# Optimization experiments

Hardware: AMD Instinct MI355X
Metric: run time of the kernel (lower is better)

The kernel has to match this reference:

```python
import jax, jax.numpy as jnp
import numpy as np

DIM = 1024
N_HEADS = 16
HEAD_DIM = DIM // N_HEADS


def setup_inputs() -> dict:
    key = jax.random.key(0)
    ks = jax.random.split(key, 7)
    B, S = 2, 2048
    scale = 0.02
    return {
        "q": jax.random.normal(ks[0], (B, S, DIM), dtype=jnp.float32),
        "k": jax.random.normal(ks[1], (B, S, DIM), dtype=jnp.float32),
        "v": jax.random.normal(ks[2], (B, S, DIM), dtype=jnp.float32),
        # torch nn.Linear weights are [out_features, in_features]; y = x @ W.T
        "wq": jax.random.normal(ks[3], (DIM, DIM), dtype=jnp.float32) * scale,
        "wk": jax.random.normal(ks[4], (DIM, DIM), dtype=jnp.float32) * scale,
        "wv": jax.random.normal(ks[5], (DIM, DIM), dtype=jnp.float32) * scale,
        "wo": jax.random.normal(ks[6], (DIM, DIM), dtype=jnp.float32) * scale,
    }


def reference(q, k, v, wq, wk, wv, wo):
    B, S, _ = q.shape
    H, D = N_HEADS, HEAD_DIM
    # projections (torch Linear: x @ W.T), reshape to [B, H, S, D]
    xq = (q @ wq.T).reshape(B, S, H, D).transpose(0, 2, 1, 3)
    xk = (k @ wk.T).reshape(B, S, H, D).transpose(0, 2, 1, 3)
    xv = (v @ wv.T).reshape(B, S, H, D).transpose(0, 2, 1, 3)
    # scaled dot-product attention with causal mask
    scores = jnp.einsum("bhqd,bhkd->bhqk", xq, xk) / jnp.sqrt(jnp.float32(D))
    causal = jnp.tril(jnp.ones((S, S), dtype=bool))
    scores = jnp.where(causal, scores, -jnp.inf)
    attn = jax.nn.softmax(scores.astype(jnp.float32), axis=-1).astype(xq.dtype)
    # dropout prob = 0.0 (eval-mode / deterministic reference)
    out = jnp.einsum("bhqk,bhkd->bhqd", attn, xv)
    out = out.transpose(0, 2, 1, 3).reshape(B, S, H * D)
    return out @ wo.T
```

## Files before the change

### kernel.cpp

```cpp
#include <hip/hip_runtime.h>
#include <hip/hip_bf16.h>
#include <stdint.h>


typedef short s16x8 __attribute__((ext_vector_type(8)));
typedef float f32x4 __attribute__((ext_vector_type(4)));

#define MFMA_BF16 __builtin_amdgcn_mfma_f32_16x16x32_bf16

static __device__ __forceinline__ unsigned short f2bf(float f) {
    union { float f; unsigned u; } x{f};
    unsigned r = x.u + 0x7fff + ((x.u >> 16) & 1);
    return (unsigned short)(r >> 16);
}
static __device__ __forceinline__ unsigned pk2h(float a, float b) {
    __hip_bfloat162 h = __float22bfloat162_rn(float2{a, b});
    return *(unsigned*)&h;
}

static __device__ __forceinline__ void ald16(unsigned short* lds, const unsigned short* g) {
    __builtin_amdgcn_global_load_lds(
        (const __attribute__((address_space(1))) unsigned int*)g,
        (__attribute__((address_space(3))) unsigned int*)lds, 16, 0, 0);
}

#define QSCL 0.18033688f

__global__ __launch_bounds__(256) void convert_all_kernel(
        const float* __restrict__ q, const float* __restrict__ k,
        const float* __restrict__ v,
        const float* __restrict__ wq, const float* __restrict__ wk,
        const float* __restrict__ wv, const float* __restrict__ wo,
        unsigned short* __restrict__ dst) {
    const size_t idx = ((size_t)blockIdx.x * 256 + threadIdx.x) * 8;
    const int region = (int)(idx >> 22);
    const float* src;
    size_t off;
    if (region == 0)      { src = q; off = idx; }
    else if (region == 1) { src = k; off = idx & 4194303; }
    else if (region == 2) { src = v; off = idx & 4194303; }
    else {
        const int wsel = (int)((idx >> 20) & 3);
        src = wsel == 0 ? wq : wsel == 1 ? wk : wsel == 2 ? wv : wo;
        off = idx & 1048575;
    }
    const float4* p = (const float4*)(src + off);
    float4 a = p[0], b = p[1];
    uint4 u;
    u.x = pk2h(a.x, a.y); u.y = pk2h(a.z, a.w);
    u.z = pk2h(b.x, b.y); u.w = pk2h(b.z, b.w);
    *(uint4*)(dst + idx) = u;
}

__global__ __launch_bounds__(256) void wconvert_kernel(
        const float* __restrict__ wq, const float* __restrict__ wk,
        const float* __restrict__ wv, const float* __restrict__ wo,
        unsigned short* __restrict__ Wb) {
    const size_t idx = ((size_t)blockIdx.x * 256 + threadIdx.x) * 8;
    const int region = (int)(idx >> 20);
    const size_t off = idx & 1048575;
    const float* src = region == 0 ? wq : region == 1 ? wk : region == 2 ? wv : wo;
    const float4* p = (const float4*)(src + off);
    float4 a = p[0], b = p[1];
    uint4 u;
    u.x = pk2h(a.x, a.y); u.y = pk2h(a.z, a.w);
    u.z = pk2h(b.x, b.y); u.w = pk2h(b.z, b.w);
    *(uint4*)(Wb + idx) = u;
}

__global__ __launch_bounds__(256) void proj3b_kernel(
        const unsigned short* __restrict__ Qb, const unsigned short* __restrict__ Kb,
        const unsigned short* __restrict__ Vb, const unsigned short* __restrict__ Wb,
        unsigned short* __restrict__ Xq, unsigned short* __restrict__ Xk,
        unsigned short* __restrict__ Xvt) {
    constexpr int Kd = 1024;
    __shared__ union {
        struct { unsigned short A[3][128 * 32]; unsigned short B[3][128 * 32]; } s;
        unsigned short T[4 * 64 * 68];
    } sm;

    const int z = blockIdx.z;
    const unsigned short* A  = z == 0 ? Qb : z == 1 ? Kb : Vb;
    const unsigned short* Bw = Wb + (size_t)z * 1048576;

    const int t = threadIdx.x;
    const int m0 = blockIdx.x * 128, n0 = blockIdx.y * 128;
    const int w = t >> 6, lane = t & 63, fr = lane & 15, g = lane >> 4;
    const int wm = (w >> 1) * 64, wn = (w & 1) * 64;
    const int brow = t >> 2;
    const int cB = (t & 3) ^ ((t >> 3) & 3);
    const int sB = g ^ ((fr >> 1) & 3);

    f32x4 acc[4][4] = {};

    auto STAGE = [&](int p, int kk) {
        ald16(sm.s.A[p] + (size_t)w * 512,        A  + (size_t)(m0 + brow) * Kd + kk + cB * 8);
        ald16(sm.s.A[p] + 2048 + (size_t)w * 512, A  + (size_t)(m0 + 64 + brow) * Kd + kk + cB * 8);
        ald16(sm.s.B[p] + (size_t)w * 512,        Bw + (size_t)(n0 + brow) * Kd + kk + cB * 8);
        ald16(sm.s.B[p] + 2048 + (size_t)w * 512, Bw + (size_t)(n0 + 64 + brow) * Kd + kk + cB * 8);
    };

    STAGE(0, 0);
    STAGE(1, 32);
    int bi = 0, nb = 2;

    for (int k0 = 0; k0 < Kd; k0 += 32) {
        if (k0 < Kd - 64) {
            STAGE(nb, k0 + 64);
            asm volatile("s_waitcnt vmcnt(8)" ::: "memory");
        } else if (k0 < Kd - 32) {
            asm volatile("s_waitcnt vmcnt(4)" ::: "memory");
        } else {
            asm volatile("s_waitcnt vmcnt(0)" ::: "memory");
        }
        __builtin_amdgcn_s_barrier();
        asm volatile("" ::: "memory");

        s16x8 af[4], bfv[4];
#pragma unroll
        for (int mi = 0; mi < 4; ++mi)
            af[mi] = *(const s16x8*)(sm.s.A[bi] + (wm + mi * 16 + fr) * 32 + sB * 8);
#pragma unroll
        for (int ni = 0; ni < 4; ++ni)
            bfv[ni] = *(const s16x8*)(sm.s.B[bi] + (wn + ni * 16 + fr) * 32 + sB * 8);
#pragma unroll
        for (int mi = 0; mi < 4; ++mi)
#pragma unroll
            for (int ni = 0; ni < 4; ++ni)
                acc[mi][ni] = MFMA_BF16(af[mi], bfv[ni], acc[mi][ni], 0, 0, 0);

        asm volatile("" ::: "memory");
        __builtin_amdgcn_s_barrier();
        bi = bi == 2 ? 0 : bi + 1;
        nb = nb == 2 ? 0 : nb + 1;
    }

    if (z != 2) {
        unsigned short* C = z ? Xk : Xq;
        const float osc = z == 0 ? QSCL : 1.0f;
#pragma unroll
        for (int mi = 0; mi < 4; ++mi)
#pragma unroll
            for (int ni = 0; ni < 4; ++ni)
#pragma unroll
                for (int reg = 0; reg < 4; ++reg)
                    C[(size_t)(m0 + wm + mi * 16 + g * 4 + reg) * 1024 +
                      n0 + wn + ni * 16 + fr] = f2bf(acc[mi][ni][reg] * osc);
    } else {
        unsigned short* T = sm.T + w * (64 * 68);
#pragma unroll
        for (int mi = 0; mi < 4; ++mi)
#pragma unroll
            for (int ni = 0; ni < 4; ++ni) {
                uint2 u;
                u.x = pk2h(acc[mi][ni][0], acc[mi][ni][1]);
                u.y = pk2h(acc[mi][ni][2], acc[mi][ni][3]);
                *(uint2*)(T + (ni * 16 + fr) * 68 + mi * 16 + g * 4) = u;
            }
        __asm__ __volatile__("" ::: "memory");
#pragma unroll
        for (int pass = 0; pass < 8; ++pass) {
            const int row = pass * 8 + (lane >> 3);
            const int chk = lane & 7;
            uint4 d = *(const uint4*)(T + row * 68 + chk * 8);
            *(uint4*)(Xvt + (size_t)(n0 + wn + row) * 4096 + m0 + wm + chk * 8) = d;
        }
    }
}

__global__ __launch_bounds__(256) void proj3_kernel(
        const float* __restrict__ q, const float* __restrict__ k, const float* __restrict__ v,
        const unsigned short* __restrict__ Wb,
        unsigned short* __restrict__ Xq, unsigned short* __restrict__ Xk,
        unsigned short* __restrict__ Xvt) {
    constexpr int Kd = 1024;
    __shared__ unsigned short lsA[128 * 40];
    __shared__ unsigned short lsB[128 * 32];
    __shared__ unsigned short Tls[4 * 64 * 68];

    const int z = blockIdx.z;
    const float* A = z == 0 ? q : z == 1 ? k : v;
    const unsigned short* Bw = Wb + (size_t)z * 1048576;

    const int t = threadIdx.x;
    const int m0 = blockIdx.x * 128, n0 = blockIdx.y * 128;
    const int w = t >> 6, lane = t & 63, fr = lane & 15, g = lane >> 4, fq = g * 8;
    const int wm = (w >> 1) * 64, wn = (w & 1) * 64;
    const int ar = t >> 1, ac = (t & 1) * 16;
    const int brow = t >> 2;
    const int cB = (t & 3) ^ ((t >> 3) & 3);
    const int sB = g ^ ((fr >> 1) & 3);

    f32x4 acc[4][4] = {};

    for (int k0 = 0; k0 < Kd; k0 += 32) {
        ald16(lsB + (size_t)w * 512,        Bw + (size_t)(n0 + brow) * Kd + k0 + cB * 8);
        ald16(lsB + 2048 + (size_t)w * 512, Bw + (size_t)(n0 + 64 + brow) * Kd + k0 + cB * 8);
        {
            const float4* pa = (const float4*)(A + (size_t)(m0 + ar) * Kd + k0 + ac);
            float4 a0 = pa[0], a1 = pa[1], a2 = pa[2], a3 = pa[3];
            uint4 u0, u1;
            u0.x = pk2h(a0.x, a0.y); u0.y = pk2h(a0.z, a0.w);
            u0.z = pk2h(a1.x, a1.y); u0.w = pk2h(a1.z, a1.w);
            u1.x = pk2h(a2.x, a2.y); u1.y = pk2h(a2.z, a2.w);
            u1.z = pk2h(a3.x, a3.y); u1.w = pk2h(a3.z, a3.w);
            *(uint4*)(lsA + ar * 40 + ac)     = u0;
            *(uint4*)(lsA + ar * 40 + ac + 8) = u1;
        }
        __syncthreads();

        s16x8 af[4], bfv[4];
#pragma unroll
        for (int mi = 0; mi < 4; ++mi)
            af[mi] = *(const s16x8*)(lsA + (wm + mi * 16 + fr) * 40 + fq);
#pragma unroll
        for (int ni = 0; ni < 4; ++ni)
            bfv[ni] = *(const s16x8*)(lsB + (wn + ni * 16 + fr) * 32 + sB * 8);
#pragma unroll
        for (int mi = 0; mi < 4; ++mi)
#pragma unroll
            for (int ni = 0; ni < 4; ++ni)
                acc[mi][ni] = MFMA_BF16(af[mi], bfv[ni], acc[mi][ni], 0, 0, 0);
        __syncthreads();
    }

    if (z != 2) {
        unsigned short* C = z ? Xk : Xq;
        const float osc = z == 0 ? QSCL : 1.0f;
#pragma unroll
        for (int mi = 0; mi < 4; ++mi)
#pragma unroll
            for (int ni = 0; ni < 4; ++ni)
#pragma unroll
                for (int reg = 0; reg < 4; ++reg)
                    C[(size_t)(m0 + wm + mi * 16 + g * 4 + reg) * 1024 +
                      n0 + wn + ni * 16 + fr] = f2bf(acc[mi][ni][reg] * osc);
    } else {
        unsigned short* T = Tls + w * (64 * 68);
#pragma unroll
        for (int mi = 0; mi < 4; ++mi)
#pragma unroll
            for (int ni = 0; ni < 4; ++ni) {
                uint2 u;
                u.x = pk2h(acc[mi][ni][0], acc[mi][ni][1]);
                u.y = pk2h(acc[mi][ni][2], acc[mi][ni][3]);
                *(uint2*)(T + (ni * 16 + fr) * 68 + mi * 16 + g * 4) = u;
            }
        __asm__ __volatile__("" ::: "memory");
#pragma unroll
        for (int pass = 0; pass < 8; ++pass) {
            const int row = pass * 8 + (lane >> 3);
            const int chk = lane & 7;
            uint4 d = *(const uint4*)(T + row * 68 + chk * 8);
            *(uint4*)(Xvt + (size_t)(n0 + wn + row) * 4096 + m0 + wm + chk * 8) = d;
        }
    }
}

static __device__ __forceinline__ void slab_tail(
        const f32x4 sf[4], int kt, int qt, int qrow, float& l_part,
        f32x4* oacc, unsigned short* Pw, const s16x8 vf[4][2], int fr, int g) {
    float e[4][4];
    const bool diag = (kt == qt);
#pragma unroll
    for (int m16 = 0; m16 < 4; ++m16)
#pragma unroll
        for (int r = 0; r < 4; ++r) {
            float x = sf[m16][r];
            if (diag) {
                const int keyg = kt * 64 + m16 * 16 + g * 4 + r;
                x = (keyg <= qrow) ? x : -1e30f;
            }
            const float ee = exp2f(x);
            e[m16][r] = ee;
            l_part += ee;
        }
#pragma unroll
    for (int m16 = 0; m16 < 4; ++m16) {
        uint2 u;
        u.x = pk2h(e[m16][0], e[m16][1]);
        u.y = pk2h(e[m16][2], e[m16][3]);
        const int ch = 2 * m16 + (g >> 1);
        *(uint2*)(Pw + fr * 64 + ((ch ^ (fr & 7)) * 8) + (g & 1) * 4) = u;
    }
    __asm__ __volatile__("" ::: "memory");
    s16x8 pf0 = *(const s16x8*)(Pw + fr * 64 + ((g ^ (fr & 7)) * 8));
    s16x8 pf1 = *(const s16x8*)(Pw + fr * 64 + (((4 + g) ^ (fr & 7)) * 8));
#pragma unroll
    for (int m16 = 0; m16 < 4; ++m16) {
        oacc[m16] = MFMA_BF16(vf[m16][0], pf0, oacc[m16], 0, 0, 0);
        oacc[m16] = MFMA_BF16(vf[m16][1], pf1, oacc[m16], 0, 0, 0);
    }
    __asm__ __volatile__("" ::: "memory");
}

__global__ __launch_bounds__(256, 2) void flash_attn_kernel(
        const unsigned short* __restrict__ Xq, const unsigned short* __restrict__ Xk,
        const unsigned short* __restrict__ Xvt, unsigned short* __restrict__ Oa) {
    __shared__ unsigned short Kls[64 * 64];
    __shared__ unsigned short Vls[64 * 64];
    __shared__ unsigned short Pls[4][16 * 64];

    const int t = threadIdx.x;
    const int bh = blockIdx.x;
    const int j = blockIdx.y;
    const int b = bh >> 4, h = bh & 15;
    const size_t rbase = (size_t)b * 2048;
    const int cbase = h * 64;

    const int w = t >> 6, lane = t & 63, fr = lane & 15, g = lane >> 4, fq = g * 8;
    const int qtH = 31 - j, qtL = j;
    const int qrowH = qtH * 64 + w * 16 + fr;
    const int qrowL = qtL * 64 + w * 16 + fr;

    const unsigned short* qpH = Xq + (rbase + qrowH) * 1024 + cbase;
    s16x8 qfH0 = *(const s16x8*)(qpH + fq);
    s16x8 qfH1 = *(const s16x8*)(qpH + 32 + fq);
    const unsigned short* qpL = Xq + (rbase + qrowL) * 1024 + cbase;
    s16x8 qfL0 = *(const s16x8*)(qpL + fq);
    s16x8 qfL1 = *(const s16x8*)(qpL + 32 + fq);

    float lH = 0.f, lL = 0.f;
    f32x4 oH[4] = {}, oL[4] = {};

    const int r0 = w * 16 + (lane >> 3), r1 = r0 + 8;
    const int s8 = lane & 7;
    const int c0 = s8 ^ (r0 & 7), c1 = s8 ^ (r1 & 7);
    const unsigned short* kbase = Xk + rbase * 1024 + cbase;
    const size_t vrow0 = (size_t)(cbase + r0) * 4096 + rbase + c0 * 8;
    const size_t vrow1 = (size_t)(cbase + r1) * 4096 + rbase + c1 * 8;

    uint4 kA, kB, vA, vB;
    kA = *(const uint4*)(kbase + (size_t)r0 * 1024 + c0 * 8);
    kB = *(const uint4*)(kbase + (size_t)r1 * 1024 + c1 * 8);
    vA = *(const uint4*)(Xvt + vrow0);
    vB = *(const uint4*)(Xvt + vrow1);

    for (int kt = 0; kt <= qtH; ++kt) {
        *(uint4*)(Kls + (w * 16) * 64 + lane * 8)     = kA;
        *(uint4*)(Kls + (w * 16 + 8) * 64 + lane * 8) = kB;
        *(uint4*)(Vls + (w * 16) * 64 + lane * 8)     = vA;
        *(uint4*)(Vls + (w * 16 + 8) * 64 + lane * 8) = vB;
        __syncthreads();

        if (kt < qtH) {
            const unsigned short* ks = kbase + (size_t)(kt + 1) * 65536;
            kA = *(const uint4*)(ks + (size_t)r0 * 1024 + c0 * 8);
            kB = *(const uint4*)(ks + (size_t)r1 * 1024 + c1 * 8);
            vA = *(const uint4*)(Xvt + vrow0 + (size_t)(kt + 1) * 64);
            vB = *(const uint4*)(Xvt + vrow1 + (size_t)(kt + 1) * 64);
        }

        const bool doL = (kt <= qtL);

        s16x8 kf[4][2], vf[4][2];
#pragma unroll
        for (int m16 = 0; m16 < 4; ++m16) {
            const int rr = m16 * 16 + fr;
            kf[m16][0] = *(const s16x8*)(Kls + rr * 64 + ((g ^ (fr & 7)) * 8));
            kf[m16][1] = *(const s16x8*)(Kls + rr * 64 + (((4 + g) ^ (fr & 7)) * 8));
            vf[m16][0] = *(const s16x8*)(Vls + rr * 64 + ((g ^ (fr & 7)) * 8));
            vf[m16][1] = *(const s16x8*)(Vls + rr * 64 + (((4 + g) ^ (fr & 7)) * 8));
        }

        f32x4 sH[4], sL[4];
#pragma unroll
        for (int m16 = 0; m16 < 4; ++m16) {
            f32x4 zz = {};
            zz = MFMA_BF16(kf[m16][0], qfH0, zz, 0, 0, 0);
            sH[m16] = MFMA_BF16(kf[m16][1], qfH1, zz, 0, 0, 0);
        }
        if (doL) {
#pragma unroll
            for (int m16 = 0; m16 < 4; ++m16) {
                f32x4 zz = {};
                zz = MFMA_BF16(kf[m16][0], qfL0, zz, 0, 0, 0);
                sL[m16] = MFMA_BF16(kf[m16][1], qfL1, zz, 0, 0, 0);
            }
        }
        slab_tail(sH, kt, qtH, qrowH, lH, oH, &Pls[w][0], vf, fr, g);
        if (doL)
            slab_tail(sL, kt, qtL, qrowL, lL, oL, &Pls[w][0], vf, fr, g);
        __syncthreads();
    }

    lH += __shfl_xor(lH, 16, 64);
    lH += __shfl_xor(lH, 32, 64);
    lL += __shfl_xor(lL, 16, 64);
    lL += __shfl_xor(lL, 32, 64);
    const float invH = 1.0f / lH, invL = 1.0f / lL;
#pragma unroll
    for (int m16 = 0; m16 < 4; ++m16) {
        uint2 u;
        u.x = pk2h(oH[m16][0] * invH, oH[m16][1] * invH);
        u.y = pk2h(oH[m16][2] * invH, oH[m16][3] * invH);
        *(uint2*)(Oa + (rbase + qrowH) * 1024 + cbase + m16 * 16 + g * 4) = u;
        uint2 u2;
        u2.x = pk2h(oL[m16][0] * invL, oL[m16][1] * invL);
        u2.y = pk2h(oL[m16][2] * invL, oL[m16][3] * invL);
        *(uint2*)(Oa + (rbase + qrowL) * 1024 + cbase + m16 * 16 + g * 4) = u2;
    }
}

__global__ __launch_bounds__(256) void outproj_kernel(
        const unsigned short* __restrict__ Oa, const unsigned short* __restrict__ Wo,
        float* __restrict__ out) {
    constexpr int Kd = 1024;
    __shared__ unsigned short lsA[3][64 * 32];
    __shared__ unsigned short lsB[3][128 * 32];

    const int t = threadIdx.x;
    const int m0 = blockIdx.x * 64, n0 = blockIdx.y * 128;
    const int w = t >> 6, lane = t & 63, fr = lane & 15, g = lane >> 4;
    const int wm = (w >> 1) * 32, wn = (w & 1) * 64;
    const int brow = t >> 2;
    const int cB = (t & 3) ^ ((t >> 3) & 3);
    const int sB = g ^ ((fr >> 1) & 3);

    f32x4 acc[2][4] = {};

    auto STAGE = [&](int p, int kk) {
        ald16(lsA[p] + (size_t)w * 512,        Oa + (size_t)(m0 + brow) * Kd + kk + cB * 8);
        ald16(lsB[p] + (size_t)w * 512,        Wo + (size_t)(n0 + brow) * Kd + kk + cB * 8);
        ald16(lsB[p] + 2048 + (size_t)w * 512, Wo + (size_t)(n0 + 64 + brow) * Kd + kk + cB * 8);
    };

    STAGE(0, 0);
    STAGE(1, 32);
    int bi = 0, nb = 2;

    for (int k0 = 0; k0 < Kd; k0 += 32) {
        if (k0 < Kd - 64) {
            STAGE(nb, k0 + 64);
            asm volatile("s_waitcnt vmcnt(6)" ::: "memory");
        } else if (k0 < Kd - 32) {
            asm volatile("s_waitcnt vmcnt(3)" ::: "memory");
        } else {
            asm volatile("s_waitcnt vmcnt(0)" ::: "memory");
        }
        __builtin_amdgcn_s_barrier();
        asm volatile("" ::: "memory");

        s16x8 af[2], bfv[4];
#pragma unroll
        for (int mi = 0; mi < 2; ++mi)
            af[mi] = *(const s16x8*)(lsA[bi] + (wm + mi * 16 + fr) * 32 + sB * 8);
#pragma unroll
        for (int ni = 0; ni < 4; ++ni)
            bfv[ni] = *(const s16x8*)(lsB[bi] + (wn + ni * 16 + fr) * 32 + sB * 8);
#pragma unroll
        for (int mi = 0; mi < 2; ++mi)
#pragma unroll
            for (int ni = 0; ni < 4; ++ni)
                acc[mi][ni] = MFMA_BF16(af[mi], bfv[ni], acc[mi][ni], 0, 0, 0);

        asm volatile("" ::: "memory");
        __builtin_amdgcn_s_barrier();
        bi = bi == 2 ? 0 : bi + 1;
        nb = nb == 2 ? 0 : nb + 1;
    }

#pragma unroll
    for (int mi = 0; mi < 2; ++mi)
#pragma unroll
        for (int ni = 0; ni < 4; ++ni)
#pragma unroll
            for (int reg = 0; reg < 4; ++reg)
                out[(size_t)(m0 + wm + mi * 16 + g * 4 + reg) * 1024 +
                    n0 + wn + ni * 16 + fr] = acc[mi][ni][reg];
}

extern "C" void kernel_launch(void* const* d_in, const int* in_sizes, int n_in,
                              void* d_out, int out_size, void* d_ws, size_t ws_size,
                              hipStream_t stream) {
    const float* q  = (const float*)d_in[0];
    const float* k  = (const float*)d_in[1];
    const float* v  = (const float*)d_in[2];
    const float* wq = (const float*)d_in[3];
    const float* wk = (const float*)d_in[4];
    const float* wv = (const float*)d_in[5];
    const float* wo = (const float*)d_in[6];
    float* out = (float*)d_out;

    if (ws_size >= (size_t)64 * 1024 * 1024) {
        unsigned short* base = (unsigned short*)d_ws;
        unsigned short* Qb  = base;
        unsigned short* Kb  = base + 4194304;
        unsigned short* Vb  = base + 8388608;
        unsigned short* Wb  = base + 12582912;
        unsigned short* Xq  = base + 16777216;
        unsigned short* Xk  = base + 20971520;
        unsigned short* Xvt = base + 25165824;
        unsigned short* Oa  = base + 29360128;

        convert_all_kernel<<<8192, 256, 0, stream>>>(q, k, v, wq, wk, wv, wo, base);
        proj3b_kernel<<<dim3(32, 8, 3), 256, 0, stream>>>(Qb, Kb, Vb, Wb, Xq, Xk, Xvt);
        flash_attn_kernel<<<dim3(32, 16), 256, 0, stream>>>(Xq, Xk, Xvt, Oa);
        outproj_kernel<<<dim3(64, 8), 256, 0, stream>>>(Oa, Wb + 3145728, out);
    } else {
        unsigned short* Wb  = (unsigned short*)d_ws;
        unsigned short* Xq  = Wb  + 4194304;
        unsigned short* Xk  = Xq  + 4194304;
        unsigned short* Xvt = Xk  + 4194304;
        unsigned short* Oa  = Xvt + 4194304;

        wconvert_kernel<<<2048, 256, 0, stream>>>(wq, wk, wv, wo, Wb);
        proj3_kernel<<<dim3(32, 8, 3), 256, 0, stream>>>(q, k, v, Wb, Xq, Xk, Xvt);
        flash_attn_kernel<<<dim3(32, 16), 256, 0, stream>>>(Xq, Xk, Xvt, Oa);
        outproj_kernel<<<dim3(64, 8), 256, 0, stream>>>(Oa, Wb + 3145728, out);
    }
}
```

Before: 201.9 us.

## Load K/V fragments directly from global into registers, drop LDS staging

Removes the shared-memory staging of K and V tiles and the per-tile block barriers. Each wave now loads its MFMA operand fragments straight from global memory, double-buffering K fragments in registers across a two-tile unrolled loop. The four waves in a block each fetch the same K/V data, so redundant global/L2 traffic rises and register pressure grows, in exchange for no LDS round trips or syncs. Also switches exp2f to the raw hardware exp2 builtin.

```diff
diff --git a/kernel.cpp b/kernel.cpp
--- a/kernel.cpp
+++ b/kernel.cpp
@@ -271,7 +271,7 @@
                 const int keyg = kt * 64 + m16 * 16 + g * 4 + r;
                 x = (keyg <= qrow) ? x : -1e30f;
             }
-            const float ee = exp2f(x);
+            const float ee = __builtin_amdgcn_exp2f(x);
             e[m16][r] = ee;
             l_part += ee;
         }
@@ -297,8 +297,6 @@
 __global__ __launch_bounds__(256, 2) void flash_attn_kernel(
         const unsigned short* __restrict__ Xq, const unsigned short* __restrict__ Xk,
         const unsigned short* __restrict__ Xvt, unsigned short* __restrict__ Oa) {
-    __shared__ unsigned short Kls[64 * 64];
-    __shared__ unsigned short Vls[64 * 64];
     __shared__ unsigned short Pls[4][16 * 64];
 
     const int t = threadIdx.x;
@@ -323,66 +321,70 @@
     float lH = 0.f, lL = 0.f;
     f32x4 oH[4] = {}, oL[4] = {};
 
-    const int r0 = w * 16 + (lane >> 3), r1 = r0 + 8;
-    const int s8 = lane & 7;
-    const int c0 = s8 ^ (r0 & 7), c1 = s8 ^ (r1 & 7);
     const unsigned short* kbase = Xk + rbase * 1024 + cbase;
-    const size_t vrow0 = (size_t)(cbase + r0) * 4096 + rbase + c0 * 8;
-    const size_t vrow1 = (size_t)(cbase + r1) * 4096 + rbase + c1 * 8;
-
-    uint4 kA, kB, vA, vB;
-    kA = *(const uint4*)(kbase + (size_t)r0 * 1024 + c0 * 8);
-    kB = *(const uint4*)(kbase + (size_t)r1 * 1024 + c1 * 8);
-    vA = *(const uint4*)(Xvt + vrow0);
-    vB = *(const uint4*)(Xvt + vrow1);
-
-    for (int kt = 0; kt <= qtH; ++kt) {
-        *(uint4*)(Kls + (w * 16) * 64 + lane * 8)     = kA;
-        *(uint4*)(Kls + (w * 16 + 8) * 64 + lane * 8) = kB;
-        *(uint4*)(Vls + (w * 16) * 64 + lane * 8)     = vA;
-        *(uint4*)(Vls + (w * 16 + 8) * 64 + lane * 8) = vB;
-        __syncthreads();
-
-        if (kt < qtH) {
-            const unsigned short* ks = kbase + (size_t)(kt + 1) * 65536;
-            kA = *(const uint4*)(ks + (size_t)r0 * 1024 + c0 * 8);
-            kB = *(const uint4*)(ks + (size_t)r1 * 1024 + c1 * 8);
-            vA = *(const uint4*)(Xvt + vrow0 + (size_t)(kt + 1) * 64);
-            vB = *(const uint4*)(Xvt + vrow1 + (size_t)(kt + 1) * 64);
-        }
-
-        const bool doL = (kt <= qtL);
-
-        s16x8 kf[4][2], vf[4][2];
-#pragma unroll
-        for (int m16 = 0; m16 < 4; ++m16) {
-            const int rr = m16 * 16 + fr;
-            kf[m16][0] = *(const s16x8*)(Kls + rr * 64 + ((g ^ (fr & 7)) * 8));
-            kf[m16][1] = *(const s16x8*)(Kls + rr * 64 + (((4 + g) ^ (fr & 7)) * 8));
-            vf[m16][0] = *(const s16x8*)(Vls + rr * 64 + ((g ^ (fr & 7)) * 8));
-            vf[m16][1] = *(const s16x8*)(Vls + rr * 64 + (((4 + g) ^ (fr & 7)) * 8));
-        }
-
-        f32x4 sH[4], sL[4];
-#pragma unroll
-        for (int m16 = 0; m16 < 4; ++m16) {
-            f32x4 zz = {};
-            zz = MFMA_BF16(kf[m16][0], qfH0, zz, 0, 0, 0);
-            sH[m16] = MFMA_BF16(kf[m16][1], qfH1, zz, 0, 0, 0);
-        }
-        if (doL) {
-#pragma unroll
-            for (int m16 = 0; m16 < 4; ++m16) {
-                f32x4 zz = {};
-                zz = MFMA_BF16(kf[m16][0], qfL0, zz, 0, 0, 0);
-                sL[m16] = MFMA_BF16(kf[m16][1], qfL1, zz, 0, 0, 0);
-            }
-        }
-        slab_tail(sH, kt, qtH, qrowH, lH, oH, &Pls[w][0], vf, fr, g);
-        if (doL)
-            slab_tail(sL, kt, qtL, qrowL, lL, oL, &Pls[w][0], vf, fr, g);
-        __syncthreads();
-    }
+    unsigned koff[4], voff[4];
+#pragma unroll
+    for (int m16 = 0; m16 < 4; ++m16) {
+        const int rr = m16 * 16 + fr;
+        koff[m16] = (unsigned)(rr * 1024 + g * 8);
+        voff[m16] = (unsigned)((cbase + rr) * 4096) + (unsigned)rbase + (unsigned)(g * 8);
+    }
+
+#define LOADK(dst, kti) do {                                                  \
+    const unsigned kb_ = (unsigned)(kti) * 65536u;                            \
+    _Pragma("unroll")                                                         \
+    for (int m_ = 0; m_ < 4; ++m_) {                                          \
+        dst[m_][0] = *(const s16x8*)(kbase + kb_ + koff[m_]);                 \
+        dst[m_][1] = *(const s16x8*)(kbase + kb_ + koff[m_] + 32);            \
+    } } while (0)
+
+#define LOADV(dst, kti) do {                                                  \
+    const unsigned vb_ = (unsigned)(kti) * 64u;                               \
+    _Pragma("unroll")                                                         \
+    for (int m_ = 0; m_ < 4; ++m_) {                                          \
+        dst[m_][0] = *(const s16x8*)(Xvt + vb_ + voff[m_]);                   \
+        dst[m_][1] = *(const s16x8*)(Xvt + vb_ + voff[m_] + 32);              \
+    } } while (0)
+
+#define TILE(kf, kti) do {                                                    \
+    const int kt_ = (kti);                                                    \
+    const bool doL_ = (kt_ <= qtL);                                           \
+    f32x4 sH[4], sL[4];                                                       \
+    _Pragma("unroll")                                                         \
+    for (int m_ = 0; m_ < 4; ++m_) {                                          \
+        f32x4 zz = {};                                                        \
+        zz = MFMA_BF16(kf[m_][0], qfH0, zz, 0, 0, 0);                         \
+        sH[m_] = MFMA_BF16(kf[m_][1], qfH1, zz, 0, 0, 0);                     \
+    }                                                                         \
+    if (doL_) {                                                               \
+        _Pragma("unroll")                                                     \
+        for (int m_ = 0; m_ < 4; ++m_) {                                      \
+            f32x4 zz = {};                                                    \
+            zz = MFMA_BF16(kf[m_][0], qfL0, zz, 0, 0, 0);                     \
+            sL[m_] = MFMA_BF16(kf[m_][1], qfL1, zz, 0, 0, 0);                 \
+        }                                                                     \
+    }                                                                         \
+    slab_tail(sH, kt_, qtH, qrowH, lH, oH, &Pls[w][0], vf, fr, g);            \
+    if (doL_)                                                                 \
+        slab_tail(sL, kt_, qtL, qrowL, lL, oL, &Pls[w][0], vf, fr, g);        \
+    } while (0)
+
+    s16x8 kf0[4][2], kf1[4][2], vf[4][2];
+    LOADK(kf0, 0);
+
+    for (int kt = 0; kt <= qtH; kt += 2) {
+        if (kt + 1 <= qtH) LOADK(kf1, kt + 1);
+        LOADV(vf, kt);
+        TILE(kf0, kt);
+        if (kt + 1 <= qtH) {
+            if (kt + 2 <= qtH) LOADK(kf0, kt + 2);
+            LOADV(vf, kt + 1);
+            TILE(kf1, kt + 1);
+        }
+    }
+#undef LOADK
+#undef LOADV
+#undef TILE
 
     lH += __shfl_xor(lH, 16, 64);
     lH += __shfl_xor(lH, 32, 64);
```

Result: slower. 264.8 us (+31.2%).

## Split paired causal q-tiles into separate blocks with double-buffered K/V LDS

Applied to the files above, without the earlier changes.

Each flash-attention block now handles one 64-row query tile instead of pairing a high and low tile for load balance. The grid doubles to 32x32 and the occupancy hint rises to 4 blocks per CU. K/V shared tiles are double-buffered so each iteration needs one barrier instead of two, and exp2f is swapped for the hardware exp2 builtin. The cost is uneven per-block work under the causal mask, which now relies on the scheduler ordering long blocks first, plus more LDS per block.

```diff
diff --git a/kernel.cpp b/kernel.cpp
--- a/kernel.cpp
+++ b/kernel.cpp
@@ -271,7 +271,7 @@
                 const int keyg = kt * 64 + m16 * 16 + g * 4 + r;
                 x = (keyg <= qrow) ? x : -1e30f;
             }
-            const float ee = exp2f(x);
+            const float ee = __builtin_amdgcn_exp2f(x);
             e[m16][r] = ee;
             l_part += ee;
         }
@@ -294,34 +294,29 @@
     __asm__ __volatile__("" ::: "memory");
 }
 
-__global__ __launch_bounds__(256, 2) void flash_attn_kernel(
+__global__ __launch_bounds__(256, 4) void flash_attn_kernel(
         const unsigned short* __restrict__ Xq, const unsigned short* __restrict__ Xk,
         const unsigned short* __restrict__ Xvt, unsigned short* __restrict__ Oa) {
-    __shared__ unsigned short Kls[64 * 64];
-    __shared__ unsigned short Vls[64 * 64];
+    __shared__ unsigned short Kls[2][64 * 64];
+    __shared__ unsigned short Vls[2][64 * 64];
     __shared__ unsigned short Pls[4][16 * 64];
 
     const int t = threadIdx.x;
     const int bh = blockIdx.x;
-    const int j = blockIdx.y;
+    const int qt = 31 - blockIdx.y;
     const int b = bh >> 4, h = bh & 15;
     const size_t rbase = (size_t)b * 2048;
     const int cbase = h * 64;
 
     const int w = t >> 6, lane = t & 63, fr = lane & 15, g = lane >> 4, fq = g * 8;
-    const int qtH = 31 - j, qtL = j;
-    const int qrowH = qtH * 64 + w * 16 + fr;
-    const int qrowL = qtL * 64 + w * 16 + fr;
-
-    const unsigned short* qpH = Xq + (rbase + qrowH) * 1024 + cbase;
-    s16x8 qfH0 = *(const s16x8*)(qpH + fq);
-    s16x8 qfH1 = *(const s16x8*)(qpH + 32 + fq);
-    const unsigned short* qpL = Xq + (rbase + qrowL) * 1024 + cbase;
-    s16x8 qfL0 = *(const s16x8*)(qpL + fq);
-    s16x8 qfL1 = *(const s16x8*)(qpL + 32 + fq);
-
-    float lH = 0.f, lL = 0.f;
-    f32x4 oH[4] = {}, oL[4] = {};
+    const int qrow = qt * 64 + w * 16 + fr;
+
+    const unsigned short* qp = Xq + (rbase + qrow) * 1024 + cbase;
+    s16x8 qf0 = *(const s16x8*)(qp + fq);
+    s16x8 qf1 = *(const s16x8*)(qp + 32 + fq);
+
+    float l = 0.f;
+    f32x4 o[4] = {};
 
     const int r0 = w * 16 + (lane >> 3), r1 = r0 + 8;
     const int s8 = lane & 7;
@@ -330,20 +325,21 @@
     const size_t vrow0 = (size_t)(cbase + r0) * 4096 + rbase + c0 * 8;
     const size_t vrow1 = (size_t)(cbase + r1) * 4096 + rbase + c1 * 8;
 
-    uint4 kA, kB, vA, vB;
-    kA = *(const uint4*)(kbase + (size_t)r0 * 1024 + c0 * 8);
-    kB = *(const uint4*)(kbase + (size_t)r1 * 1024 + c1 * 8);
-    vA = *(const uint4*)(Xvt + vrow0);
-    vB = *(const uint4*)(Xvt + vrow1);
-
-    for (int kt = 0; kt <= qtH; ++kt) {
-        *(uint4*)(Kls + (w * 16) * 64 + lane * 8)     = kA;
-        *(uint4*)(Kls + (w * 16 + 8) * 64 + lane * 8) = kB;
-        *(uint4*)(Vls + (w * 16) * 64 + lane * 8)     = vA;
-        *(uint4*)(Vls + (w * 16 + 8) * 64 + lane * 8) = vB;
-        __syncthreads();
-
-        if (kt < qtH) {
+    uint4 kA = *(const uint4*)(kbase + (size_t)r0 * 1024 + c0 * 8);
+    uint4 kB = *(const uint4*)(kbase + (size_t)r1 * 1024 + c1 * 8);
+    uint4 vA = *(const uint4*)(Xvt + vrow0);
+    uint4 vB = *(const uint4*)(Xvt + vrow1);
+
+    *(uint4*)(Kls[0] + (w * 16) * 64 + lane * 8)     = kA;
+    *(uint4*)(Kls[0] + (w * 16 + 8) * 64 + lane * 8) = kB;
+    *(uint4*)(Vls[0] + (w * 16) * 64 + lane * 8)     = vA;
+    *(uint4*)(Vls[0] + (w * 16 + 8) * 64 + lane * 8) = vB;
+    __syncthreads();
+
+    for (int kt = 0; kt <= qt; ++kt) {
+        const int cur = kt & 1;
+
+        if (kt < qt) {
             const unsigned short* ks = kbase + (size_t)(kt + 1) * 65536;
             kA = *(const uint4*)(ks + (size_t)r0 * 1024 + c0 * 8);
             kB = *(const uint4*)(ks + (size_t)r1 * 1024 + c1 * 8);
@@ -351,54 +347,44 @@
             vB = *(const uint4*)(Xvt + vrow1 + (size_t)(kt + 1) * 64);
         }
 
-        const bool doL = (kt <= qtL);
-
         s16x8 kf[4][2], vf[4][2];
 #pragma unroll
         for (int m16 = 0; m16 < 4; ++m16) {
             const int rr = m16 * 16 + fr;
-            kf[m16][0] = *(const s16x8*)(Kls + rr * 64 + ((g ^ (fr & 7)) * 8));
-            kf[m16][1] = *(const s16x8*)(Kls + rr * 64 + (((4 + g) ^ (fr & 7)) * 8));
-            vf[m16][0] = *(const s16x8*)(Vls + rr * 64 + ((g ^ (fr & 7)) * 8));
-            vf[m16][1] = *(const s16x8*)(Vls + rr * 64 + (((4 + g) ^ (fr & 7)) * 8));
-        }
-
-        f32x4 sH[4], sL[4];
+            kf[m16][0] = *(const s16x8*)(Kls[cur] + rr * 64 + ((g ^ (fr & 7)) * 8));
+            kf[m16][1] = *(const s16x8*)(Kls[cur] + rr * 64 + (((4 + g) ^ (fr & 7)) * 8));
+            vf[m16][0] = *(const s16x8*)(Vls[cur] + rr * 64 + ((g ^ (fr & 7)) * 8));
+            vf[m16][1] = *(const s16x8*)(Vls[cur] + rr * 64 + (((4 + g) ^ (fr & 7)) * 8));
+        }
+
+        f32x4 s[4];
 #pragma unroll
         for (int m16 = 0; m16 < 4; ++m16) {
             f32x4 zz = {};
-            zz = MFMA_BF16(kf[m16][0], qfH0, zz, 0, 0, 0);
-            sH[m16] = MFMA_BF16(kf[m16][1], qfH1, zz, 0, 0, 0);
-        }
-        if (doL) {
-#pragma unroll
-            for (int m16 = 0; m16 < 4; ++m16) {
-                f32x4 zz = {};
-                zz = MFMA_BF16(kf[m16][0], qfL0, zz, 0, 0, 0);
-                sL[m16] = MFMA_BF16(kf[m16][1], qfL1, zz, 0, 0, 0);
-            }
-        }
-        slab_tail(sH, kt, qtH, qrowH, lH, oH, &Pls[w][0], vf, fr, g);
-        if (doL)
-            slab_tail(sL, kt, qtL, qrowL, lL, oL, &Pls[w][0], vf, fr, g);
-        __syncthreads();
-    }
-
-    lH += __shfl_xor(lH, 16, 64);
-    lH += __shfl_xor(lH, 32, 64);
-    lL += __shfl_xor(lL, 16, 64);
-    lL += __shfl_xor(lL, 32, 64);
-    const float invH = 1.0f / lH, invL = 1.0f / lL;
+            zz = MFMA_BF16(kf[m16][0], qf0, zz, 0, 0, 0);
+            s[m16] = MFMA_BF16(kf[m16][1], qf1, zz, 0, 0, 0);
+        }
+        slab_tail(s, kt, qt, qrow, l, o, &Pls[w][0], vf, fr, g);
+
+        if (kt < qt) {
+            const int nxt = cur ^ 1;
+            *(uint4*)(Kls[nxt] + (w * 16) * 64 + lane * 8)     = kA;
+            *(uint4*)(Kls[nxt] + (w * 16 + 8) * 64 + lane * 8) = kB;
+            *(uint4*)(Vls[nxt] + (w * 16) * 64 + lane * 8)     = vA;
+            *(uint4*)(Vls[nxt] + (w * 16 + 8) * 64 + lane * 8) = vB;
+            __syncthreads();
+        }
+    }
+
+    l += __shfl_xor(l, 16, 64);
+    l += __shfl_xor(l, 32, 64);
+    const float inv = 1.0f / l;
 #pragma unroll
     for (int m16 = 0; m16 < 4; ++m16) {
         uint2 u;
-        u.x = pk2h(oH[m16][0] * invH, oH[m16][1] * invH);
-        u.y = pk2h(oH[m16][2] * invH, oH[m16][3] * invH);
-        *(uint2*)(Oa + (rbase + qrowH) * 1024 + cbase + m16 * 16 + g * 4) = u;
-        uint2 u2;
-        u2.x = pk2h(oL[m16][0] * invL, oL[m16][1] * invL);
-        u2.y = pk2h(oL[m16][2] * invL, oL[m16][3] * invL);
-        *(uint2*)(Oa + (rbase + qrowL) * 1024 + cbase + m16 * 16 + g * 4) = u2;
+        u.x = pk2h(o[m16][0] * inv, o[m16][1] * inv);
+        u.y = pk2h(o[m16][2] * inv, o[m16][3] * inv);
+        *(uint2*)(Oa + (rbase + qrow) * 1024 + cbase + m16 * 16 + g * 4) = u;
     }
 }
 
@@ -495,7 +481,7 @@
 
         convert_all_kernel<<<8192, 256, 0, stream>>>(q, k, v, wq, wk, wv, wo, base);
         proj3b_kernel<<<dim3(32, 8, 3), 256, 0, stream>>>(Qb, Kb, Vb, Wb, Xq, Xk, Xvt);
-        flash_attn_kernel<<<dim3(32, 16), 256, 0, stream>>>(Xq, Xk, Xvt, Oa);
+        flash_attn_kernel<<<dim3(32, 32), 256, 0, stream>>>(Xq, Xk, Xvt, Oa);
         outproj_kernel<<<dim3(64, 8), 256, 0, stream>>>(Oa, Wb + 3145728, out);
     } else {
         unsigned short* Wb  = (unsigned short*)d_ws;
@@ -506,7 +492,7 @@
 
         wconvert_kernel<<<2048, 256, 0, stream>>>(wq, wk, wv, wo, Wb);
         proj3_kernel<<<dim3(32, 8, 3), 256, 0, stream>>>(q, k, v, Wb, Xq, Xk, Xvt);
-        flash_attn_kernel<<<dim3(32, 16), 256, 0, stream>>>(Xq, Xk, Xvt, Oa);
+        flash_attn_kernel<<<dim3(32, 32), 256, 0, stream>>>(Xq, Xk, Xvt, Oa);
         outproj_kernel<<<dim3(64, 8), 256, 0, stream>>>(Oa, Wb + 3145728, out);
     }
 }
```

New measurement: 200.3 us. No clear change (-0.8%).

## Double-buffer K/V tiles in LDS, raise MFMA priority, use native exp2

Applied to the files above, without the earlier changes.

Turns the single K/V LDS tile into a ping-pong buffer. The next tile is written into the alternate buffer after compute, which removes one of the two barriers per key tile. It also wraps the MFMA sections in s_setprio to favour matrix issue across waves, and swaps exp2f for the raw hardware exp2 intrinsic. In exchange, LDS use grows by 16KB per block, which could limit occupancy at two blocks per CU, and the raw exp2 skips denormal handling.

```diff
diff --git a/kernel.cpp b/kernel.cpp
--- a/kernel.cpp
+++ b/kernel.cpp
@@ -271,7 +271,7 @@
                 const int keyg = kt * 64 + m16 * 16 + g * 4 + r;
                 x = (keyg <= qrow) ? x : -1e30f;
             }
-            const float ee = exp2f(x);
+            const float ee = __builtin_amdgcn_exp2f(x);
             e[m16][r] = ee;
             l_part += ee;
         }
@@ -286,19 +286,21 @@
     __asm__ __volatile__("" ::: "memory");
     s16x8 pf0 = *(const s16x8*)(Pw + fr * 64 + ((g ^ (fr & 7)) * 8));
     s16x8 pf1 = *(const s16x8*)(Pw + fr * 64 + (((4 + g) ^ (fr & 7)) * 8));
+    __builtin_amdgcn_s_setprio(1);
 #pragma unroll
     for (int m16 = 0; m16 < 4; ++m16) {
         oacc[m16] = MFMA_BF16(vf[m16][0], pf0, oacc[m16], 0, 0, 0);
         oacc[m16] = MFMA_BF16(vf[m16][1], pf1, oacc[m16], 0, 0, 0);
     }
+    __builtin_amdgcn_s_setprio(0);
     __asm__ __volatile__("" ::: "memory");
 }
 
 __global__ __launch_bounds__(256, 2) void flash_attn_kernel(
         const unsigned short* __restrict__ Xq, const unsigned short* __restrict__ Xk,
         const unsigned short* __restrict__ Xvt, unsigned short* __restrict__ Oa) {
-    __shared__ unsigned short Kls[64 * 64];
-    __shared__ unsigned short Vls[64 * 64];
+    __shared__ unsigned short Kls[2][64 * 64];
+    __shared__ unsigned short Vls[2][64 * 64];
     __shared__ unsigned short Pls[4][16 * 64];
 
     const int t = threadIdx.x;
@@ -330,18 +332,19 @@
     const size_t vrow0 = (size_t)(cbase + r0) * 4096 + rbase + c0 * 8;
     const size_t vrow1 = (size_t)(cbase + r1) * 4096 + rbase + c1 * 8;
 
-    uint4 kA, kB, vA, vB;
-    kA = *(const uint4*)(kbase + (size_t)r0 * 1024 + c0 * 8);
-    kB = *(const uint4*)(kbase + (size_t)r1 * 1024 + c1 * 8);
-    vA = *(const uint4*)(Xvt + vrow0);
-    vB = *(const uint4*)(Xvt + vrow1);
+    uint4 kA = *(const uint4*)(kbase + (size_t)r0 * 1024 + c0 * 8);
+    uint4 kB = *(const uint4*)(kbase + (size_t)r1 * 1024 + c1 * 8);
+    uint4 vA = *(const uint4*)(Xvt + vrow0);
+    uint4 vB = *(const uint4*)(Xvt + vrow1);
+
+    *(uint4*)(Kls[0] + (w * 16) * 64 + lane * 8)     = kA;
+    *(uint4*)(Kls[0] + (w * 16 + 8) * 64 + lane * 8) = kB;
+    *(uint4*)(Vls[0] + (w * 16) * 64 + lane * 8)     = vA;
+    *(uint4*)(Vls[0] + (w * 16 + 8) * 64 + lane * 8) = vB;
+    __syncthreads();
 
     for (int kt = 0; kt <= qtH; ++kt) {
-        *(uint4*)(Kls + (w * 16) * 64 + lane * 8)     = kA;
-        *(uint4*)(Kls + (w * 16 + 8) * 64 + lane * 8) = kB;
-        *(uint4*)(Vls + (w * 16) * 64 + lane * 8)     = vA;
-        *(uint4*)(Vls + (w * 16 + 8) * 64 + lane * 8) = vB;
-        __syncthreads();
+        const int cur = kt & 1;
 
         if (kt < qtH) {
             const unsigned short* ks = kbase + (size_t)(kt + 1) * 65536;
@@ -357,13 +360,14 @@
 #pragma unroll
         for (int m16 = 0; m16 < 4; ++m16) {
             const int rr = m16 * 16 + fr;
-            kf[m16][0] = *(const s16x8*)(Kls + rr * 64 + ((g ^ (fr & 7)) * 8));
-            kf[m16][1] = *(const s16x8*)(Kls + rr * 64 + (((4 + g) ^ (fr & 7)) * 8));
-            vf[m16][0] = *(const s16x8*)(Vls + rr * 64 + ((g ^ (fr & 7)) * 8));
-            vf[m16][1] = *(const s16x8*)(Vls + rr * 64 + (((4 + g) ^ (fr & 7)) * 8));
+            kf[m16][0] = *(const s16x8*)(Kls[cur] + rr * 64 + ((g ^ (fr & 7)) * 8));
+            kf[m16][1] = *(const s16x8*)(Kls[cur] + rr * 64 + (((4 + g) ^ (fr & 7)) * 8));
+            vf[m16][0] = *(const s16x8*)(Vls[cur] + rr * 64 + ((g ^ (fr & 7)) * 8));
+            vf[m16][1] = *(const s16x8*)(Vls[cur] + rr * 64 + (((4 + g) ^ (fr & 7)) * 8));
         }
 
         f32x4 sH[4], sL[4];
+        __builtin_amdgcn_s_setprio(1);
 #pragma unroll
         for (int m16 = 0; m16 < 4; ++m16) {
             f32x4 zz = {};
@@ -378,10 +382,20 @@
                 sL[m16] = MFMA_BF16(kf[m16][1], qfL1, zz, 0, 0, 0);
             }
         }
+        __builtin_amdgcn_s_setprio(0);
+
         slab_tail(sH, kt, qtH, qrowH, lH, oH, &Pls[w][0], vf, fr, g);
         if (doL)
             slab_tail(sL, kt, qtL, qrowL, lL, oL, &Pls[w][0], vf, fr, g);
-        __syncthreads();
+
+        if (kt < qtH) {
+            const int nxt = cur ^ 1;
+            *(uint4*)(Kls[nxt] + (w * 16) * 64 + lane * 8)     = kA;
+            *(uint4*)(Kls[nxt] + (w * 16 + 8) * 64 + lane * 8) = kB;
+            *(uint4*)(Vls[nxt] + (w * 16) * 64 + lane * 8)     = vA;
+            *(uint4*)(Vls[nxt] + (w * 16 + 8) * 64 + lane * 8) = vB;
+            __syncthreads();
+        }
     }
 
     lH += __shfl_xor(lH, 16, 64);
```

After: 197.5 us. -2.2%, faster.
